# Performance work log

Hardware: AMD Instinct MI355X
Metric: run time of the kernel (lower is better)

The kernel has to match this reference:

```python
import jax, jax.numpy as jnp
import numpy as np

B, N, D, H = 32, 64, 64, 4
E = 4 * D
HD = E // H
EPS = 1e-10
TAU = 1.0


def _ln(x, g, b, eps=1e-5):
    m = x.mean(-1, keepdims=True)
    v = ((x - m) ** 2).mean(-1, keepdims=True)
    return (x - m) * jax.lax.rsqrt(v + eps) * g + b


def setup_inputs() -> dict:
    key = jax.random.key(0)
    ks = jax.random.split(key, 8)
    x = jax.random.normal(ks[0], (B, N, D), jnp.float32)
    A = jax.random.normal(ks[1], (B, N, N, 2 * D), jnp.float32)
    attn_mask = jax.random.randint(ks[2], (B, N, N), 0, 2).astype(jnp.int32)
    gumbel_u = jax.random.uniform(ks[3], (B, N, H, N), jnp.float32, minval=1e-6, maxval=1.0)
    in_proj_w = (jax.random.normal(ks[4], (3 * E, E), jnp.float32) * (E ** -0.5))
    in_proj_b = jnp.zeros((3 * E,), jnp.float32)
    w1 = jax.random.normal(ks[5], (HD, HD), jnp.float32) * (HD ** -0.5)
    b1 = jnp.zeros((HD,), jnp.float32)
    w2 = jax.random.normal(ks[6], (1, HD), jnp.float32) * (HD ** -0.5)
    b2 = jnp.zeros((1,), jnp.float32)
    return dict(x=x, A=A, attn_mask=attn_mask, gumbel_u=gumbel_u,
                ln_node_g=jnp.ones((D,), jnp.float32), ln_node_b=jnp.zeros((D,), jnp.float32),
                ln_edge_g=jnp.ones((2 * D,), jnp.float32), ln_edge_b=jnp.zeros((2 * D,), jnp.float32),
                in_proj_w=in_proj_w, in_proj_b=in_proj_b, w1=w1, b1=b1, w2=w2, b2=b2)


def reference(x, A, attn_mask, gumbel_u, ln_node_g, ln_node_b, ln_edge_g, ln_edge_b,
              in_proj_w, in_proj_b, w1, b1, w2, b2):
    b, n, d = x.shape
    e = 4 * d
    hd = e // H
    mask = attn_mask.astype(x.dtype)                      # (b, target, neighbor), 1/0
    ped = (mask.sum(-1) > 0).astype(x.dtype)[..., None]   # (b, n, 1)
    xn = _ln(x, ln_node_g, ln_node_b) * ped
    An = _ln(A, ln_edge_g, ln_edge_b) * jnp.transpose(mask, (0, 2, 1))[..., None]
    # broadcast concat: (b, neighbor, target, 4d)
    xneigh = jnp.broadcast_to(xn[:, :, None, :], (b, n, n, d))
    xtarg = jnp.broadcast_to(xn[:, None, :, :], (b, n, n, d))
    A4 = jnp.concatenate([xneigh, xtarg, An], axis=-1)
    Ap = jnp.transpose(A4, (0, 2, 1, 3))                  # (b, target, neighbor, 4d)
    # in-projection (torch MHA layout: rows [q; k; v])
    qkv = jnp.einsum('btme,fe->btmf', Ap, in_proj_w) + in_proj_b
    q, k, v = jnp.split(qkv, 3, axis=-1)
    q = q.reshape(b, n, n, H, hd) * (hd ** -0.5)
    k = k.reshape(b, n, n, H, hd)
    v = v.reshape(b, n, n, H, hd)
    scores = jnp.einsum('btjhd,btkhd->bthjk', q, k)       # per-target neighborhood attention
    m3 = mask[:, :, :, None] * mask[:, :, None, :]        # (b, t, j, k)
    w = jax.nn.softmax(scores, axis=-1) * m3[:, :, None, :, :]
    w = w / (w.sum(-1, keepdims=True) + EPS)
    A2 = jnp.einsum('bthjk,btkhd->bthjd', w, v)           # (b, target, head, neighbor, hd)
    hmid = jax.nn.relu(jnp.einsum('bthjd,od->bthjo', A2, w1) + b1)
    logits = (jnp.einsum('bthjo,xo->bthjx', hmid, w2) + b2)[..., 0]  # (b, t, h, j)
    em = jax.nn.softmax(logits, axis=-1) * mask[:, :, None, :]
    em = em / (em.sum(-1, keepdims=True) + EPS)
    g = -jnp.log(-jnp.log(gumbel_u + EPS) + EPS)
    sampled = jax.nn.softmax((jnp.log(em + EPS) + g) / TAU, axis=-1)
    return em, sampled
```

## Files before the change

kernel.cpp:

```cpp
#include <hip/hip_runtime.h>
#include <hip/hip_bf16.h>
#include <math.h>


typedef __attribute__((ext_vector_type(8))) short short8;
typedef __attribute__((ext_vector_type(4))) short short4v;
typedef __attribute__((ext_vector_type(4))) float f32x4;

__device__ __forceinline__ short f2b(float f) {
  return (short)__builtin_bit_cast(unsigned short, __float2bfloat16(f));
}

#define ROW16(nt, i) ((((nt) >> 1) * 32) + (((i) >> 2) * 8) + (((nt) & 1) * 4) + ((i) & 3))
__device__ __forceinline__ int phiA(int r) { return r * 136 + (r >> 3) * 8; }
__device__ __forceinline__ int phiB(int r) { return r * 72 + (r >> 3) * 8; }

#define OFF_B0 17504
#define OFF_F  36128
#define LDS_BYTES 40736

__global__ __launch_bounds__(256) void k_node_ln(
    const float* __restrict__ x, const int* __restrict__ mask,
    const float* __restrict__ g, const float* __restrict__ bb,
    float* __restrict__ xn) {
  int tid = threadIdx.x;
  int row = blockIdx.x * 4 + (tid >> 6);
  int lane = tid & 63;
  float v = x[row * 64 + lane];
  float s = v;
#pragma unroll
  for (int m = 1; m < 64; m <<= 1) s += __shfl_xor(s, m, 64);
  float mean = s * (1.0f / 64.0f);
  float dv = v - mean;
  float s2 = dv * dv;
#pragma unroll
  for (int m = 1; m < 64; m <<= 1) s2 += __shfl_xor(s2, m, 64);
  float rstd = rsqrtf(s2 * (1.0f / 64.0f) + 1e-5f);
  float msum = (float)mask[row * 64 + lane];
#pragma unroll
  for (int m = 1; m < 64; m <<= 1) msum += __shfl_xor(msum, m, 64);
  float ped = (msum > 0.0f) ? 1.0f : 0.0f;
  xn[row * 64 + lane] = (dv * rstd * g[lane] + bb[lane]) * ped;
}

__global__ __launch_bounds__(256) void k_t12(
    const float* __restrict__ xn, const float* __restrict__ W,
    const float* __restrict__ bias, float* __restrict__ T1s, float* __restrict__ T2) {
  __shared__ __align__(16) float sx[8 * 64];
  int tid = threadIdx.x;
  int r0 = blockIdx.x * 8;
#pragma unroll
  for (int u = 0; u < 2; ++u) {
    int idx = tid + 256 * u;
    sx[idx] = xn[r0 * 64 + idx];
  }
  __syncthreads();
#pragma unroll
  for (int ff = 0; ff < 3; ++ff) {
    int f = tid + 256 * ff;
    float acc1[8], acc2[8];
#pragma unroll
    for (int r = 0; r < 8; ++r) { acc1[r] = 0.f; acc2[r] = 0.f; }
    for (int e4 = 0; e4 < 64; e4 += 4) {
      float4 wa = *(const float4*)&W[f * 256 + e4];
      float4 wb = *(const float4*)&W[f * 256 + 64 + e4];
#pragma unroll
      for (int r = 0; r < 8; ++r) {
        float4 xv = *(const float4*)&sx[r * 64 + e4];
        acc1[r] += wa.x * xv.x + wa.y * xv.y + wa.z * xv.z + wa.w * xv.w;
        acc2[r] += wb.x * xv.x + wb.y * xv.y + wb.z * xv.z + wb.w * xv.w;
      }
    }
    float bv = bias[f];
    int p = f >> 8, hh = (f >> 6) & 3, dcol = f & 63;
#pragma unroll
    for (int r = 0; r < 8; ++r) {
      int m = r0 + r;
      int bb2 = m >> 6, mm = m & 63;
      int wv_ = mm >> 4;
      int lane, reg;
      if (p == 0) {
        lane = ((dcol >> 3) & 3) * 16 + (mm & 15);
        reg  = ((dcol >> 5) * 2 + ((dcol >> 2) & 1)) * 4 + (dcol & 3);
      } else if (p == 1) {
        lane = ((dcol >> 2) & 3) * 16 + (mm & 15);
        reg  = (dcol >> 4) * 4 + (dcol & 3);
      } else {
        lane = ((mm >> 2) & 3) * 16 + (dcol & 15);
        reg  = (dcol >> 4) * 4 + (mm & 3);
      }
      T1s[(size_t)((((bb2 * 3 + p) * 4 + hh) * 4 + wv_) * 64 + lane) * 16 + reg] =
          acc1[r];
      T2[m * 768 + f] = acc2[r] + bv;
    }
  }
}

__global__ __launch_bounds__(256) void k_wb(const float* __restrict__ W,
                                            const float* __restrict__ w1,
                                            short* __restrict__ Wb,
                                            short* __restrict__ w1b) {
  int idx = blockIdx.x * 256 + threadIdx.x;
  if (idx < 12288) {
    int f = idx >> 4, gi = idx & 15;
    const float* src = &W[(size_t)f * 256 + 128 + gi * 8];
    short8 o;
#pragma unroll
    for (int i = 0; i < 8; ++i) o[i] = f2b(src[i]);
    *(short8*)&Wb[f * 128 + gi * 8] = o;
  } else if (idx < 12288 + 512) {
    int g2 = idx - 12288;
    int f = g2 >> 3, gi = g2 & 7;
    const float* src = &w1[f * 64 + gi * 8];
    short8 o;
#pragma unroll
    for (int i = 0; i < 8; ++i) o[i] = f2b(src[i]);
    *(short8*)&w1b[f * 64 + gi * 8] = o;
  }
}

__global__ __launch_bounds__(256) void k_main(
    const float* __restrict__ A, const int* __restrict__ mask,
    const float* __restrict__ gu, const float* __restrict__ leg,
    const float* __restrict__ leb, const float* __restrict__ b1g,
    const float* __restrict__ w2g, const float* __restrict__ b2g,
    const float* __restrict__ T1s, const float* __restrict__ T2,
    const short* __restrict__ Wb, const short* __restrict__ w1b,
    float* __restrict__ out) {
  __shared__ __align__(16) unsigned char smem[LDS_BYTES];
  short* sWc = (short*)smem;
  float* sF  = (float*)(smem + OFF_F);

  int tid = threadIdx.x;
  int bid0 = blockIdx.x;
  int wg = (bid0 & 7) * 128 + (bid0 >> 3);
  int tq = wg & 31, b = wg >> 5;
  int t0 = tq * 2;
  int bt0 = b * 64 + t0;
  int wave = tid >> 6, lane = tid & 63, lr = lane & 15, lh = lane >> 4;
  short* sB[2] = {(short*)(smem + OFF_B0), (short*)(smem + OFF_B0) + 4656};

  if (tid < 64) sF[384 + tid] = (float)mask[bt0 * 64 + tid];
  else if (tid < 128) sF[448 + tid - 64] = (float)mask[(bt0 + 1) * 64 + tid - 64];
  else if (tid < 192) sF[512 + tid - 128] = b1g[tid - 128];
  else sF[576 + tid - 192] = w2g[tid - 192];

  short8 af[2][4];
#pragma unroll
  for (int e = 0; e < 2; ++e) {
    int m0 = wave * 16 + lr;
    const float* Ar = A + ((size_t)((b * 64 + m0) * 64 + t0 + e)) * 128;
    float4 a4[8];
#pragma unroll
    for (int ks = 0; ks < 4; ++ks) {
      a4[2 * ks]     = *(const float4*)&Ar[ks * 32 + lh * 8];
      a4[2 * ks + 1] = *(const float4*)&Ar[ks * 32 + lh * 8 + 4];
    }
    float s = 0.f, s2 = 0.f;
#pragma unroll
    for (int q = 0; q < 8; ++q) {
      float4 u0 = a4[q];
      s += u0.x + u0.y + u0.z + u0.w;
      s2 += u0.x * u0.x + u0.y * u0.y + u0.z * u0.z + u0.w * u0.w;
    }
    s += __shfl_xor(s, 16, 64);  s += __shfl_xor(s, 32, 64);
    s2 += __shfl_xor(s2, 16, 64); s2 += __shfl_xor(s2, 32, 64);
    float mean = s * (1.0f / 128.0f);
    float var = s2 * (1.0f / 128.0f) - mean * mean;
    float rstd = rsqrtf(var + 1e-5f);
    float mv = (float)mask[(bt0 + e) * 64 + m0];
#pragma unroll
    for (int ks = 0; ks < 4; ++ks) {
      float4 g0 = *(const float4*)&leg[ks * 32 + lh * 8];
      float4 g1 = *(const float4*)&leg[ks * 32 + lh * 8 + 4];
      float4 c0 = *(const float4*)&leb[ks * 32 + lh * 8];
      float4 c1 = *(const float4*)&leb[ks * 32 + lh * 8 + 4];
      float gg[8] = {g0.x, g0.y, g0.z, g0.w, g1.x, g1.y, g1.z, g1.w};
      float cc[8] = {c0.x, c0.y, c0.z, c0.w, c1.x, c1.y, c1.z, c1.w};
      float4 u0 = a4[2 * ks], u1 = a4[2 * ks + 1];
      float vv[8] = {u0.x, u0.y, u0.z, u0.w, u1.x, u1.y, u1.z, u1.w};
#pragma unroll
      for (int i = 0; i < 8; ++i)
        af[e][ks][i] = f2b(((vv[i] - mean) * rstd * gg[i] + cc[i]) * mv);
    }
  }

  short8 qf[2][2], wf[2][2];

#pragma unroll 1
  for (int h = 0; h < 4; ++h) {
    __syncthreads();
    if (tid < 192) sF[tid] = T2[bt0 * 768 + (tid >> 6) * 256 + h * 64 + (tid & 63)];
    if (tid >= 64) {
      int i2 = tid - 64;
      sF[192 + i2] = T2[(bt0 + 1) * 768 + (i2 >> 6) * 256 + h * 64 + (i2 & 63)];
    }
#pragma unroll
    for (int u = 0; u < 4; ++u) {
      int idx = tid + 256 * u;
      int dR = idx >> 4, gi = idx & 15;
      *(short8*)&sWc[phiA(dR) + gi * 8] =
          *(const short8*)&Wb[(size_t)(h * 64 + dR) * 128 + gi * 8];
    }
    float4 t1f[4];
#pragma unroll
    for (int nt = 0; nt < 4; ++nt)
      t1f[nt] = *(const float4*)&T1s[
          (size_t)((((b * 3 + 0) * 4 + h) * 4 + wave) * 64 + lane) * 16 + nt * 4];
    __syncthreads();

    {
      f32x4 acc0[4], acc1[4];
#pragma unroll
      for (int nt = 0; nt < 4; ++nt) {
        acc0[nt][0] = t1f[nt].x; acc0[nt][1] = t1f[nt].y;
        acc0[nt][2] = t1f[nt].z; acc0[nt][3] = t1f[nt].w;
        acc1[nt] = acc0[nt];
      }
#pragma unroll
      for (int ks = 0; ks < 4; ++ks)
#pragma unroll
        for (int nt = 0; nt < 4; ++nt) {
          short8 bf = *(const short8*)&sWc[phiA(ROW16(nt, lr)) + ks * 32 + lh * 8];
          acc0[nt] = __builtin_amdgcn_mfma_f32_16x16x32_bf16(bf, af[0][ks], acc0[nt], 0, 0, 0);
          acc1[nt] = __builtin_amdgcn_mfma_f32_16x16x32_bf16(bf, af[1][ks], acc1[nt], 0, 0, 0);
        }
#pragma unroll
      for (int e = 0; e < 2; ++e) {
        const f32x4* acc = (e == 0) ? acc0 : acc1;
#pragma unroll
        for (int nt = 0; nt < 4; ++nt) {
          float4 t24 = *(const float4*)&sF[e * 192 + (nt >> 1) * 32 + (nt & 1) * 4 + lh * 8];
          float tv[4] = {t24.x, t24.y, t24.z, t24.w};
#pragma unroll
          for (int r = 0; r < 4; ++r)
            qf[e][nt >> 1][(nt & 1) * 4 + r] = f2b((acc[nt][r] + tv[r]) * 0.125f);
        }
      }
    }
    __syncthreads();
#pragma unroll
    for (int u = 0; u < 4; ++u) {
      int idx = tid + 256 * u;
      int dR = idx >> 4, gi = idx & 15;
      *(short8*)&sWc[phiA(dR) + gi * 8] =
          *(const short8*)&Wb[(size_t)(256 + h * 64 + dR) * 128 + gi * 8];
    }
#pragma unroll
    for (int nt = 0; nt < 4; ++nt)
      t1f[nt] = *(const float4*)&T1s[
          (size_t)((((b * 3 + 1) * 4 + h) * 4 + wave) * 64 + lane) * 16 + nt * 4];
    __syncthreads();

    {
      f32x4 acc0[4], acc1[4];
#pragma unroll
      for (int nt = 0; nt < 4; ++nt) {
        acc0[nt][0] = t1f[nt].x; acc0[nt][1] = t1f[nt].y;
        acc0[nt][2] = t1f[nt].z; acc0[nt][3] = t1f[nt].w;
        acc1[nt] = acc0[nt];
      }
#pragma unroll
      for (int ks = 0; ks < 4; ++ks)
#pragma unroll
        for (int nt = 0; nt < 4; ++nt) {
          short8 bf = *(const short8*)&sWc[phiA(nt * 16 + lr) + ks * 32 + lh * 8];
          acc0[nt] = __builtin_amdgcn_mfma_f32_16x16x32_bf16(bf, af[0][ks], acc0[nt], 0, 0, 0);
          acc1[nt] = __builtin_amdgcn_mfma_f32_16x16x32_bf16(bf, af[1][ks], acc1[nt], 0, 0, 0);
        }
#pragma unroll
      for (int e = 0; e < 2; ++e) {
        const f32x4* acc = (e == 0) ? acc0 : acc1;
#pragma unroll
        for (int nt = 0; nt < 4; ++nt) {
          float4 t24 = *(const float4*)&sF[e * 192 + 64 + nt * 16 + lh * 4];
          float tv[4] = {t24.x, t24.y, t24.z, t24.w};
          short4v kp;
#pragma unroll
          for (int r = 0; r < 4; ++r) kp[r] = f2b(acc[nt][r] + tv[r]);
          *(short4v*)&sB[e][phiB(wave * 16 + lr) + nt * 16 + lh * 4] = kp;
        }
      }
    }
    __syncthreads();
#pragma unroll
    for (int u = 0; u < 4; ++u) {
      int idx = tid + 256 * u;
      int dR = idx >> 4, gi = idx & 15;
      *(short8*)&sWc[phiA(dR) + gi * 8] =
          *(const short8*)&Wb[(size_t)(512 + h * 64 + dR) * 128 + gi * 8];
    }
    float4 t1fv[4];
#pragma unroll
    for (int nt = 0; nt < 4; ++nt)
      t1fv[nt] = *(const float4*)&T1s[
          (size_t)((((b * 3 + 2) * 4 + h) * 4 + wave) * 64 + lane) * 16 + nt * 4];

#pragma unroll
    for (int e = 0; e < 2; ++e) {
      f32x4 sc[4] = {};
#pragma unroll
      for (int ks = 0; ks < 2; ++ks)
#pragma unroll
        for (int nt = 0; nt < 4; ++nt) {
          short8 kf = *(const short8*)&sB[e][phiB(ROW16(nt, lr)) + ks * 32 + lh * 8];
          sc[nt] = __builtin_amdgcn_mfma_f32_16x16x32_bf16(kf, qf[e][ks], sc[nt], 0, 0, 0);
        }
      float mj = sF[384 + e * 64 + wave * 16 + lr];
      float mx = sc[0][0];
#pragma unroll
      for (int nt = 0; nt < 4; ++nt)
#pragma unroll
        for (int r = 0; r < 4; ++r) mx = fmaxf(mx, sc[nt][r]);
      mx = fmaxf(mx, __shfl_xor(mx, 16, 64));
      mx = fmaxf(mx, __shfl_xor(mx, 32, 64));
      float pv[4][4], mkv[4][4], Zf = 0.f, S = 0.f;
#pragma unroll
      for (int nt = 0; nt < 4; ++nt) {
        float4 mk4 = *(const float4*)&sF[384 + e * 64 + (nt >> 1) * 32 + (nt & 1) * 4 + lh * 8];
        float mk[4] = {mk4.x, mk4.y, mk4.z, mk4.w};
#pragma unroll
        for (int r = 0; r < 4; ++r) {
          float ev = __expf(sc[nt][r] - mx);
          pv[nt][r] = ev;
          mkv[nt][r] = mk[r];
          Zf += ev;
          S += ev * mk[r];
        }
      }
      Zf += __shfl_xor(Zf, 16, 64); Zf += __shfl_xor(Zf, 32, 64);
      S  += __shfl_xor(S, 16, 64);  S  += __shfl_xor(S, 32, 64);
      float inv = mj / (S + 1e-10f * Zf);
#pragma unroll
      for (int nt = 0; nt < 4; ++nt)
#pragma unroll
        for (int r = 0; r < 4; ++r)
          wf[e][nt >> 1][(nt & 1) * 4 + r] = f2b(pv[nt][r] * mkv[nt][r] * inv);
    }
    __syncthreads();

    {
      f32x4 acc0[4], acc1[4];
#pragma unroll
      for (int nt = 0; nt < 4; ++nt) {
        acc0[nt][0] = t1fv[nt].x; acc0[nt][1] = t1fv[nt].y;
        acc0[nt][2] = t1fv[nt].z; acc0[nt][3] = t1fv[nt].w;
        acc1[nt] = acc0[nt];
      }
#pragma unroll
      for (int ks = 0; ks < 4; ++ks)
#pragma unroll
        for (int nt = 0; nt < 4; ++nt) {
          short8 bf = *(const short8*)&sWc[phiA(nt * 16 + lr) + ks * 32 + lh * 8];
          acc0[nt] = __builtin_amdgcn_mfma_f32_16x16x32_bf16(af[0][ks], bf, acc0[nt], 0, 0, 0);
          acc1[nt] = __builtin_amdgcn_mfma_f32_16x16x32_bf16(af[1][ks], bf, acc1[nt], 0, 0, 0);
        }
#pragma unroll
      for (int e = 0; e < 2; ++e) {
        const f32x4* acc = (e == 0) ? acc0 : acc1;
#pragma unroll
        for (int nt = 0; nt < 4; ++nt) {
          float t2v = sF[e * 192 + 128 + nt * 16 + lr];
          short4v vp;
#pragma unroll
          for (int r = 0; r < 4; ++r) vp[r] = f2b(acc[nt][r] + t2v);
          *(short4v*)&sB[e][phiB(nt * 16 + lr) + wave * 16 + lh * 4] = vp;
        }
      }
    }
    __syncthreads();

#pragma unroll
    for (int e = 0; e < 2; ++e) {
      f32x4 a2[4] = {};
#pragma unroll
      for (int ks = 0; ks < 2; ++ks)
#pragma unroll
        for (int nt = 0; nt < 4; ++nt) {
          short8 vf = *(const short8*)&sB[e][phiB(ROW16(nt, lr)) + ks * 32 + lh * 8];
          a2[nt] = __builtin_amdgcn_mfma_f32_16x16x32_bf16(vf, wf[e][ks], a2[nt], 0, 0, 0);
        }
      short8 a2f[2];
#pragma unroll
      for (int nt = 0; nt < 4; ++nt)
#pragma unroll
        for (int r = 0; r < 4; ++r)
          a2f[nt >> 1][(nt & 1) * 4 + r] = f2b(a2[nt][r]);
      f32x4 hm[4] = {};
#pragma unroll
      for (int ks = 0; ks < 2; ++ks)
#pragma unroll
        for (int nt = 0; nt < 4; ++nt) {
          short8 w1f = *(const short8*)&w1b[ROW16(nt, lr) * 64 + ks * 32 + lh * 8];
          hm[nt] = __builtin_amdgcn_mfma_f32_16x16x32_bf16(w1f, a2f[ks], hm[nt], 0, 0, 0);
        }
      float pp_ = 0.f;
#pragma unroll
      for (int nt = 0; nt < 4; ++nt) {
        float4 b14 = *(const float4*)&sF[512 + (nt >> 1) * 32 + (nt & 1) * 4 + lh * 8];
        float4 w24 = *(const float4*)&sF[576 + (nt >> 1) * 32 + (nt & 1) * 4 + lh * 8];
        float bb4[4] = {b14.x, b14.y, b14.z, b14.w};
        float ww4[4] = {w24.x, w24.y, w24.z, w24.w};
#pragma unroll
        for (int r = 0; r < 4; ++r)
          pp_ += fmaxf(hm[nt][r] + bb4[r], 0.f) * ww4[r];
      }
      pp_ += __shfl_xor(pp_, 16, 64);
      pp_ += __shfl_xor(pp_, 32, 64);
      if (lh == 0) sF[640 + (e * 4 + h) * 64 + wave * 16 + lr] = pp_;
    }
  }
  __syncthreads();

#pragma unroll
  for (int it = 0; it < 2; ++it) {
    int tile = it, hh = wave, j = lane;
    int btx = bt0 + tile;
    float l = sF[640 + (tile * 4 + hh) * 64 + j] + b2g[0];
    float mjv = sF[384 + tile * 64 + j];
    float mx = l;
#pragma unroll
    for (int mm = 1; mm < 64; mm <<= 1) mx = fmaxf(mx, __shfl_xor(mx, mm, 64));
    float pv = __expf(l - mx);
    float Z = pv;
#pragma unroll
    for (int mm = 1; mm < 64; mm <<= 1) Z += __shfl_xor(Z, mm, 64);
    float ep = (pv / Z) * mjv;
    float S = ep;
#pragma unroll
    for (int mm = 1; mm < 64; mm <<= 1) S += __shfl_xor(S, mm, 64);
    float em = ep / (S + 1e-10f);
    float u = gu[((size_t)btx * 4 + hh) * 64 + j];
    float gg = -__logf(-__logf(u + 1e-10f) + 1e-10f);
    float l2 = __logf(em + 1e-10f) + gg;
    float mx2 = l2;
#pragma unroll
    for (int mm = 1; mm < 64; mm <<= 1) mx2 = fmaxf(mx2, __shfl_xor(mx2, mm, 64));
    float p2 = __expf(l2 - mx2);
    float Z2 = p2;
#pragma unroll
    for (int mm = 1; mm < 64; mm <<= 1) Z2 += __shfl_xor(Z2, mm, 64);
    float smp = p2 / Z2;
    size_t o = ((size_t)btx * 4 + hh) * 64 + j;
    out[o] = em;
    out[524288 + o] = smp;
  }
}

extern "C" void kernel_launch(void* const* d_in, const int* in_sizes, int n_in,
                              void* d_out, int out_size, void* d_ws, size_t ws_size,
                              hipStream_t stream) {
  const float* x    = (const float*)d_in[0];
  const float* A    = (const float*)d_in[1];
  const int*   mask = (const int*)d_in[2];
  const float* gu   = (const float*)d_in[3];
  const float* lng  = (const float*)d_in[4];
  const float* lnb  = (const float*)d_in[5];
  const float* leg  = (const float*)d_in[6];
  const float* leb  = (const float*)d_in[7];
  const float* W    = (const float*)d_in[8];
  const float* bias = (const float*)d_in[9];
  const float* w1   = (const float*)d_in[10];
  const float* b1   = (const float*)d_in[11];
  const float* w2   = (const float*)d_in[12];
  const float* b2   = (const float*)d_in[13];
  float* out = (float*)d_out;
  float* ws  = (float*)d_ws;

  float* xn  = ws;
  float* T1s = xn + 131072;
  float* T2  = T1s + 1572864;
  short* Wb  = (short*)(T2 + 1572864);
  short* w1b = Wb + 98304;

  k_wb<<<50, 256, 0, stream>>>(W, w1, Wb, w1b);
  k_node_ln<<<512, 256, 0, stream>>>(x, mask, lng, lnb, xn);
  k_t12<<<256, 256, 0, stream>>>(xn, W, bias, T1s, T2);
  k_main<<<1024, 256, 0, stream>>>(A, mask, gu, leg, leb, b1, w2, b2,
                                   T1s, T2, Wb, w1b, out);
}
```

Baseline: 136.5 us.

## Process one target per workgroup instead of two in main kernel

The main kernel now handles a single target node per workgroup instead of two, doubling the grid to 2048 blocks and shrinking LDS use and per-thread register arrays. This should raise occupancy and parallelism. In exchange, each weight slice loaded into shared memory is reused for only one target, which doubles weight-staging traffic and barrier overhead per unit of work.

```diff
diff --git a/kernel.cpp b/kernel.cpp
--- a/kernel.cpp
+++ b/kernel.cpp
@@ -15,9 +15,9 @@
 __device__ __forceinline__ int phiA(int r) { return r * 136 + (r >> 3) * 8; }
 __device__ __forceinline__ int phiB(int r) { return r * 72 + (r >> 3) * 8; }
 
-#define OFF_B0 17504
-#define OFF_F  36128
-#define LDS_BYTES 40736
+#define OFF_B  17504
+#define OFF_F  26816
+#define LDS_BYTES 29376
 
 __global__ __launch_bounds__(256) void k_node_ln(
     const float* __restrict__ x, const int* __restrict__ mask,
@@ -129,27 +129,24 @@
     float* __restrict__ out) {
   __shared__ __align__(16) unsigned char smem[LDS_BYTES];
   short* sWc = (short*)smem;
+  short* sB  = (short*)(smem + OFF_B);
   float* sF  = (float*)(smem + OFF_F);
 
   int tid = threadIdx.x;
   int bid0 = blockIdx.x;
-  int wg = (bid0 & 7) * 128 + (bid0 >> 3);
-  int tq = wg & 31, b = wg >> 5;
-  int t0 = tq * 2;
-  int bt0 = b * 64 + t0;
+  int wg = (bid0 & 7) * 256 + (bid0 >> 3);
+  int t = wg & 63, b = wg >> 6;
+  int bt = b * 64 + t;
   int wave = tid >> 6, lane = tid & 63, lr = lane & 15, lh = lane >> 4;
-  short* sB[2] = {(short*)(smem + OFF_B0), (short*)(smem + OFF_B0) + 4656};
-
-  if (tid < 64) sF[384 + tid] = (float)mask[bt0 * 64 + tid];
-  else if (tid < 128) sF[448 + tid - 64] = (float)mask[(bt0 + 1) * 64 + tid - 64];
-  else if (tid < 192) sF[512 + tid - 128] = b1g[tid - 128];
-  else sF[576 + tid - 192] = w2g[tid - 192];
-
-  short8 af[2][4];
-#pragma unroll
-  for (int e = 0; e < 2; ++e) {
+
+  if (tid < 64) sF[192 + tid] = (float)mask[bt * 64 + tid];
+  else if (tid < 128) sF[256 + tid - 64] = b1g[tid - 64];
+  else if (tid < 192) sF[320 + tid - 128] = w2g[tid - 128];
+
+  short8 af[4];
+  {
     int m0 = wave * 16 + lr;
-    const float* Ar = A + ((size_t)((b * 64 + m0) * 64 + t0 + e)) * 128;
+    const float* Ar = A + ((size_t)((b * 64 + m0) * 64 + t)) * 128;
     float4 a4[8];
 #pragma unroll
     for (int ks = 0; ks < 4; ++ks) {
@@ -168,7 +165,7 @@
     float mean = s * (1.0f / 128.0f);
     float var = s2 * (1.0f / 128.0f) - mean * mean;
     float rstd = rsqrtf(var + 1e-5f);
-    float mv = (float)mask[(bt0 + e) * 64 + m0];
+    float mv = (float)mask[bt * 64 + m0];
 #pragma unroll
     for (int ks = 0; ks < 4; ++ks) {
       float4 g0 = *(const float4*)&leg[ks * 32 + lh * 8];
@@ -181,20 +178,16 @@
       float vv[8] = {u0.x, u0.y, u0.z, u0.w, u1.x, u1.y, u1.z, u1.w};
 #pragma unroll
       for (int i = 0; i < 8; ++i)
-        af[e][ks][i] = f2b(((vv[i] - mean) * rstd * gg[i] + cc[i]) * mv);
-    }
-  }
-
-  short8 qf[2][2], wf[2][2];
+        af[ks][i] = f2b(((vv[i] - mean) * rstd * gg[i] + cc[i]) * mv);
+    }
+  }
+
+  short8 qf[2], wf[2];
 
 #pragma unroll 1
   for (int h = 0; h < 4; ++h) {
     __syncthreads();
-    if (tid < 192) sF[tid] = T2[bt0 * 768 + (tid >> 6) * 256 + h * 64 + (tid & 63)];
-    if (tid >= 64) {
-      int i2 = tid - 64;
-      sF[192 + i2] = T2[(bt0 + 1) * 768 + (i2 >> 6) * 256 + h * 64 + (i2 & 63)];
-    }
+    if (tid < 192) sF[tid] = T2[bt * 768 + (tid >> 6) * 256 + h * 64 + (tid & 63)];
 #pragma unroll
     for (int u = 0; u < 4; ++u) {
       int idx = tid + 256 * u;
@@ -210,32 +203,26 @@
     __syncthreads();
 
     {
-      f32x4 acc0[4], acc1[4];
-#pragma unroll
-      for (int nt = 0; nt < 4; ++nt) {
-        acc0[nt][0] = t1f[nt].x; acc0[nt][1] = t1f[nt].y;
-        acc0[nt][2] = t1f[nt].z; acc0[nt][3] = t1f[nt].w;
-        acc1[nt] = acc0[nt];
+      f32x4 acc[4];
+#pragma unroll
+      for (int nt = 0; nt < 4; ++nt) {
+        acc[nt][0] = t1f[nt].x; acc[nt][1] = t1f[nt].y;
+        acc[nt][2] = t1f[nt].z; acc[nt][3] = t1f[nt].w;
       }
 #pragma unroll
       for (int ks = 0; ks < 4; ++ks)
 #pragma unroll
         for (int nt = 0; nt < 4; ++nt) {
           short8 bf = *(const short8*)&sWc[phiA(ROW16(nt, lr)) + ks * 32 + lh * 8];
-          acc0[nt] = __builtin_amdgcn_mfma_f32_16x16x32_bf16(bf, af[0][ks], acc0[nt], 0, 0, 0);
-          acc1[nt] = __builtin_amdgcn_mfma_f32_16x16x32_bf16(bf, af[1][ks], acc1[nt], 0, 0, 0);
-        }
-#pragma unroll
-      for (int e = 0; e < 2; ++e) {
-        const f32x4* acc = (e == 0) ? acc0 : acc1;
-#pragma unroll
-        for (int nt = 0; nt < 4; ++nt) {
-          float4 t24 = *(const float4*)&sF[e * 192 + (nt >> 1) * 32 + (nt & 1) * 4 + lh * 8];
-          float tv[4] = {t24.x, t24.y, t24.z, t24.w};
-#pragma unroll
-          for (int r = 0; r < 4; ++r)
-            qf[e][nt >> 1][(nt & 1) * 4 + r] = f2b((acc[nt][r] + tv[r]) * 0.125f);
-        }
+          acc[nt] = __builtin_amdgcn_mfma_f32_16x16x32_bf16(bf, af[ks], acc[nt], 0, 0, 0);
+        }
+#pragma unroll
+      for (int nt = 0; nt < 4; ++nt) {
+        float4 t24 = *(const float4*)&sF[(nt >> 1) * 32 + (nt & 1) * 4 + lh * 8];
+        float tv[4] = {t24.x, t24.y, t24.z, t24.w};
+#pragma unroll
+        for (int r = 0; r < 4; ++r)
+          qf[nt >> 1][(nt & 1) * 4 + r] = f2b((acc[nt][r] + tv[r]) * 0.125f);
       }
     }
     __syncthreads();
@@ -253,33 +240,27 @@
     __syncthreads();
 
     {
-      f32x4 acc0[4], acc1[4];
-#pragma unroll
-      for (int nt = 0; nt < 4; ++nt) {
-        acc0[nt][0] = t1f[nt].x; acc0[nt][1] = t1f[nt].y;
-        acc0[nt][2] = t1f[nt].z; acc0[nt][3] = t1f[nt].w;
-        acc1[nt] = acc0[nt];
+      f32x4 acc[4];
+#pragma unroll
+      for (int nt = 0; nt < 4; ++nt) {
+        acc[nt][0] = t1f[nt].x; acc[nt][1] = t1f[nt].y;
+        acc[nt][2] = t1f[nt].z; acc[nt][3] = t1f[nt].w;
       }
 #pragma unroll
       for (int ks = 0; ks < 4; ++ks)
 #pragma unroll
         for (int nt = 0; nt < 4; ++nt) {
           short8 bf = *(const short8*)&sWc[phiA(nt * 16 + lr) + ks * 32 + lh * 8];
-          acc0[nt] = __builtin_amdgcn_mfma_f32_16x16x32_bf16(bf, af[0][ks], acc0[nt], 0, 0, 0);
-          acc1[nt] = __builtin_amdgcn_mfma_f32_16x16x32_bf16(bf, af[1][ks], acc1[nt], 0, 0, 0);
-        }
-#pragma unroll
-      for (int e = 0; e < 2; ++e) {
-        const f32x4* acc = (e == 0) ? acc0 : acc1;
-#pragma unroll
-        for (int nt = 0; nt < 4; ++nt) {
-          float4 t24 = *(const float4*)&sF[e * 192 + 64 + nt * 16 + lh * 4];
-          float tv[4] = {t24.x, t24.y, t24.z, t24.w};
-          short4v kp;
-#pragma unroll
-          for (int r = 0; r < 4; ++r) kp[r] = f2b(acc[nt][r] + tv[r]);
-          *(short4v*)&sB[e][phiB(wave * 16 + lr) + nt * 16 + lh * 4] = kp;
-        }
+          acc[nt] = __builtin_amdgcn_mfma_f32_16x16x32_bf16(bf, af[ks], acc[nt], 0, 0, 0);
+        }
+#pragma unroll
+      for (int nt = 0; nt < 4; ++nt) {
+        float4 t24 = *(const float4*)&sF[64 + nt * 16 + lh * 4];
+        float tv[4] = {t24.x, t24.y, t24.z, t24.w};
+        short4v kp;
+#pragma unroll
+        for (int r = 0; r < 4; ++r) kp[r] = f2b(acc[nt][r] + tv[r]);
+        *(short4v*)&sB[phiB(wave * 16 + lr) + nt * 16 + lh * 4] = kp;
       }
     }
     __syncthreads();
@@ -296,17 +277,16 @@
       t1fv[nt] = *(const float4*)&T1s[
           (size_t)((((b * 3 + 2) * 4 + h) * 4 + wave) * 64 + lane) * 16 + nt * 4];
 
-#pragma unroll
-    for (int e = 0; e < 2; ++e) {
+    {
       f32x4 sc[4] = {};
 #pragma unroll
       for (int ks = 0; ks < 2; ++ks)
 #pragma unroll
         for (int nt = 0; nt < 4; ++nt) {
-          short8 kf = *(const short8*)&sB[e][phiB(ROW16(nt, lr)) + ks * 32 + lh * 8];
-          sc[nt] = __builtin_amdgcn_mfma_f32_16x16x32_bf16(kf, qf[e][ks], sc[nt], 0, 0, 0);
-        }
-      float mj = sF[384 + e * 64 + wave * 16 + lr];
+          short8 kf = *(const short8*)&sB[phiB(ROW16(nt, lr)) + ks * 32 + lh * 8];
+          sc[nt] = __builtin_amdgcn_mfma_f32_16x16x32_bf16(kf, qf[ks], sc[nt], 0, 0, 0);
+        }
+      float mj = sF[192 + wave * 16 + lr];
       float mx = sc[0][0];
 #pragma unroll
       for (int nt = 0; nt < 4; ++nt)
@@ -317,7 +297,7 @@
       float pv[4][4], mkv[4][4], Zf = 0.f, S = 0.f;
 #pragma unroll
       for (int nt = 0; nt < 4; ++nt) {
-        float4 mk4 = *(const float4*)&sF[384 + e * 64 + (nt >> 1) * 32 + (nt & 1) * 4 + lh * 8];
+        float4 mk4 = *(const float4*)&sF[192 + (nt >> 1) * 32 + (nt & 1) * 4 + lh * 8];
         float mk[4] = {mk4.x, mk4.y, mk4.z, mk4.w};
 #pragma unroll
         for (int r = 0; r < 4; ++r) {
@@ -335,50 +315,43 @@
       for (int nt = 0; nt < 4; ++nt)
 #pragma unroll
         for (int r = 0; r < 4; ++r)
-          wf[e][nt >> 1][(nt & 1) * 4 + r] = f2b(pv[nt][r] * mkv[nt][r] * inv);
+          wf[nt >> 1][(nt & 1) * 4 + r] = f2b(pv[nt][r] * mkv[nt][r] * inv);
     }
     __syncthreads();
 
     {
-      f32x4 acc0[4], acc1[4];
-#pragma unroll
-      for (int nt = 0; nt < 4; ++nt) {
-        acc0[nt][0] = t1fv[nt].x; acc0[nt][1] = t1fv[nt].y;
-        acc0[nt][2] = t1fv[nt].z; acc0[nt][3] = t1fv[nt].w;
-        acc1[nt] = acc0[nt];
+      f32x4 acc[4];
+#pragma unroll
+      for (int nt = 0; nt < 4; ++nt) {
+        acc[nt][0] = t1fv[nt].x; acc[nt][1] = t1fv[nt].y;
+        acc[nt][2] = t1fv[nt].z; acc[nt][3] = t1fv[nt].w;
       }
 #pragma unroll
       for (int ks = 0; ks < 4; ++ks)
 #pragma unroll
         for (int nt = 0; nt < 4; ++nt) {
           short8 bf = *(const short8*)&sWc[phiA(nt * 16 + lr) + ks * 32 + lh * 8];
-          acc0[nt] = __builtin_amdgcn_mfma_f32_16x16x32_bf16(af[0][ks], bf, acc0[nt], 0, 0, 0);
-          acc1[nt] = __builtin_amdgcn_mfma_f32_16x16x32_bf16(af[1][ks], bf, acc1[nt], 0, 0, 0);
-        }
-#pragma unroll
-      for (int e = 0; e < 2; ++e) {
-        const f32x4* acc = (e == 0) ? acc0 : acc1;
-#pragma unroll
-        for (int nt = 0; nt < 4; ++nt) {
-          float t2v = sF[e * 192 + 128 + nt * 16 + lr];
-          short4v vp;
-#pragma unroll
-          for (int r = 0; r < 4; ++r) vp[r] = f2b(acc[nt][r] + t2v);
-          *(short4v*)&sB[e][phiB(nt * 16 + lr) + wave * 16 + lh * 4] = vp;
-        }
-      }
-    }
-    __syncthreads();
-
-#pragma unroll
-    for (int e = 0; e < 2; ++e) {
+          acc[nt] = __builtin_amdgcn_mfma_f32_16x16x32_bf16(af[ks], bf, acc[nt], 0, 0, 0);
+        }
+#pragma unroll
+      for (int nt = 0; nt < 4; ++nt) {
+        float t2v = sF[128 + nt * 16 + lr];
+        short4v vp;
+#pragma unroll
+        for (int r = 0; r < 4; ++r) vp[r] = f2b(acc[nt][r] + t2v);
+        *(short4v*)&sB[phiB(nt * 16 + lr) + wave * 16 + lh * 4] = vp;
+      }
+    }
+    __syncthreads();
+
+    {
       f32x4 a2[4] = {};
 #pragma unroll
       for (int ks = 0; ks < 2; ++ks)
 #pragma unroll
         for (int nt = 0; nt < 4; ++nt) {
-          short8 vf = *(const short8*)&sB[e][phiB(ROW16(nt, lr)) + ks * 32 + lh * 8];
-          a2[nt] = __builtin_amdgcn_mfma_f32_16x16x32_bf16(vf, wf[e][ks], a2[nt], 0, 0, 0);
+          short8 vf = *(const short8*)&sB[phiB(ROW16(nt, lr)) + ks * 32 + lh * 8];
+          a2[nt] = __builtin_amdgcn_mfma_f32_16x16x32_bf16(vf, wf[ks], a2[nt], 0, 0, 0);
         }
       short8 a2f[2];
 #pragma unroll
@@ -397,8 +370,8 @@
       float pp_ = 0.f;
 #pragma unroll
       for (int nt = 0; nt < 4; ++nt) {
-        float4 b14 = *(const float4*)&sF[512 + (nt >> 1) * 32 + (nt & 1) * 4 + lh * 8];
-        float4 w24 = *(const float4*)&sF[576 + (nt >> 1) * 32 + (nt & 1) * 4 + lh * 8];
+        float4 b14 = *(const float4*)&sF[256 + (nt >> 1) * 32 + (nt & 1) * 4 + lh * 8];
+        float4 w24 = *(const float4*)&sF[320 + (nt >> 1) * 32 + (nt & 1) * 4 + lh * 8];
         float bb4[4] = {b14.x, b14.y, b14.z, b14.w};
         float ww4[4] = {w24.x, w24.y, w24.z, w24.w};
 #pragma unroll
@@ -407,17 +380,15 @@
       }
       pp_ += __shfl_xor(pp_, 16, 64);
       pp_ += __shfl_xor(pp_, 32, 64);
-      if (lh == 0) sF[640 + (e * 4 + h) * 64 + wave * 16 + lr] = pp_;
+      if (lh == 0) sF[384 + h * 64 + wave * 16 + lr] = pp_;
     }
   }
   __syncthreads();
 
-#pragma unroll
-  for (int it = 0; it < 2; ++it) {
-    int tile = it, hh = wave, j = lane;
-    int btx = bt0 + tile;
-    float l = sF[640 + (tile * 4 + hh) * 64 + j] + b2g[0];
-    float mjv = sF[384 + tile * 64 + j];
+  {
+    int hh = wave, j = lane;
+    float l = sF[384 + hh * 64 + j] + b2g[0];
+    float mjv = sF[192 + j];
     float mx = l;
 #pragma unroll
     for (int mm = 1; mm < 64; mm <<= 1) mx = fmaxf(mx, __shfl_xor(mx, mm, 64));
@@ -430,7 +401,7 @@
 #pragma unroll
     for (int mm = 1; mm < 64; mm <<= 1) S += __shfl_xor(S, mm, 64);
     float em = ep / (S + 1e-10f);
-    float u = gu[((size_t)btx * 4 + hh) * 64 + j];
+    float u = gu[((size_t)bt * 4 + hh) * 64 + j];
     float gg = -__logf(-__logf(u + 1e-10f) + 1e-10f);
     float l2 = __logf(em + 1e-10f) + gg;
     float mx2 = l2;
@@ -441,7 +412,7 @@
 #pragma unroll
     for (int mm = 1; mm < 64; mm <<= 1) Z2 += __shfl_xor(Z2, mm, 64);
     float smp = p2 / Z2;
-    size_t o = ((size_t)btx * 4 + hh) * 64 + j;
+    size_t o = ((size_t)bt * 4 + hh) * 64 + j;
     out[o] = em;
     out[524288 + o] = smp;
   }
@@ -476,6 +447,6 @@
   k_wb<<<50, 256, 0, stream>>>(W, w1, Wb, w1b);
   k_node_ln<<<512, 256, 0, stream>>>(x, mask, lng, lnb, xn);
   k_t12<<<256, 256, 0, stream>>>(xn, W, bias, T1s, T2);
-  k_main<<<1024, 256, 0, stream>>>(A, mask, gu, leg, leb, b1, w2, b2,
+  k_main<<<2048, 256, 0, stream>>>(A, mask, gu, leg, leb, b1, w2, b2,
                                    T1s, T2, Wb, w1b, out);
 }
```

Result: no change. 136.1 us (-0.3%).
